# Performance work log

Hardware: AMD Instinct MI355X
Metric: run time of the kernel (lower is better)

Reference implementation:

```python
import jax, jax.numpy as jnp
import numpy as np

LOG2PI = float(np.log(2.0 * np.pi))
BATCH = 131072
IN_FEATURES = 128
MULT = 3          # Gaussian multiplicity / Sum in_channels
CARD = 2          # first Product cardinality -> 64 features


def setup_inputs() -> dict:
    key = jax.random.key(0)
    k1, k2, k3, k4, k5 = jax.random.split(key, 5)
    x = jax.random.normal(k1, (BATCH, IN_FEATURES), dtype=jnp.float32)
    means = jax.random.normal(k2, (1, IN_FEATURES, MULT), dtype=jnp.float32)
    # stds drawn positive (torch.rand init for scale params)
    stds = jax.random.uniform(k3, (1, IN_FEATURES, MULT), dtype=jnp.float32,
                              minval=0.1, maxval=1.0)
    sum_weights = jax.random.normal(k4, (64, MULT, 1), dtype=jnp.float32)
    # randomized Product layer: fixed random permutation of the 128 features
    perm = jax.random.permutation(k5, IN_FEATURES).astype(jnp.int32)
    return {"x": x, "means": means, "stds": stds,
            "sum_weights": sum_weights, "perm": perm}


def reference(x, means, stds, sum_weights, perm):
    n = x.shape[0]
    # --- Gaussian leaf: Normal(mu, sigma).log_prob(x) -> [n, 128, 3]
    z = (x[:, :, None] - means) / stds
    lp = -0.5 * (z * z) - jnp.log(stds) - 0.5 * LOG2PI
    # --- Product(in_features=128, cardinality=2, randomize): permute features,
    # pair them up, product in log-domain = sum -> [n, 64, 3]
    lp = lp[:, perm, :]
    lp = lp.reshape(n, IN_FEATURES // CARD, CARD, MULT).sum(axis=2)
    # --- Sum(in_channels=3, in_features=64, out_channels=1): weighted
    # log-sum-exp mixture over channels with log_softmax-normalized weights
    logw = jax.nn.log_softmax(sum_weights, axis=1)          # [64, 3, 1]
    lp = jax.nn.logsumexp(lp[:, :, :, None] + logw[None], axis=2)  # [n, 64, 1]
    # --- Product(in_features=64, cardinality=64): sum all features -> [n, 1, 1]
    # (permutation before a full reduction is a no-op, so omitted)
    out = lp.sum(axis=1, keepdims=True).reshape(n, 1, 1)
    return out
```

## Files before the change

### kernel.cpp

```cpp
#include <hip/hip_runtime.h>

#define N_FEAT 128
#define ROWS   32
#define TPB    256

template<int CTRL>
__device__ __forceinline__ float dpp_xadd(float v) {
    int t = __builtin_amdgcn_update_dpp(0, __float_as_int(v), CTRL, 0xF, 0xF, true);
    return v + __int_as_float(t);
}

__device__ __forceinline__ float wave_allsum(float v) {
    v = dpp_xadd<0xB1>(v);
    v = dpp_xadd<0x4E>(v);
    v = dpp_xadd<0x141>(v);
    v = dpp_xadd<0x140>(v);
#if __has_builtin(__builtin_amdgcn_permlane16_swap)
    {
        auto p = __builtin_amdgcn_permlane16_swap(__float_as_uint(v), __float_as_uint(v), false, false);
        v = __uint_as_float(p[0]) + __uint_as_float(p[1]);
    }
#else
    v += __int_as_float(__builtin_amdgcn_ds_swizzle(__float_as_int(v), 0x401F));
#endif
    {
        auto p = __builtin_amdgcn_permlane32_swap(__float_as_uint(v), __float_as_uint(v), false, false);
        v = __uint_as_float(p[0]) + __uint_as_float(p[1]);
    }
    return v;
}

__global__ __launch_bounds__(TPB, 6)
void spn_fused(const float* __restrict__ x,
               const float* __restrict__ means,
               const float* __restrict__ stds,
               const float* __restrict__ sumw,
               const int* __restrict__ perm,
               float* __restrict__ out, int n) {
    __shared__ float sx[ROWS * N_FEAT];

    const float NHALF_LOG2E = -0.7213475204444817f;
    const float LN2     = 0.6931471805599453f;
    const float LOG2PI_ = 1.8378770664093453f;
    const float LOG2E   = 1.4426950408889634f;

    const int tid  = threadIdx.x;
    const int lane = tid & 63;
    const int wv   = tid >> 6;

    const int ntiles = n / ROWS;

    auto issue_tile = [&](int t) {
        const float* g0 = x + (size_t)t * (ROWS * N_FEAT);
#pragma unroll
        for (int it = 0; it < 4; ++it) {
            const int chunk = it * 4 + wv;
            __builtin_amdgcn_global_load_lds(
                (const __attribute__((address_space(1))) unsigned*)(g0 + chunk * 256 + lane * 4),
                (__attribute__((address_space(3))) unsigned*)(sx + chunk * 256),
                16, 0, 0);
        }
    };

    int tile  = blockIdx.x;
    bool have = tile < ntiles;
    if (have) issue_tile(tile);

    const int g  = lane;
    const int p0 = perm[2 * g], p1 = perm[2 * g + 1];
    const float w0 = sumw[g * 3 + 0], w1 = sumw[g * 3 + 1], w2 = sumw[g * 3 + 2];
    const float wmx = fmaxf(w0, fmaxf(w1, w2));
    const float lse = wmx + logf(expf(w0 - wmx) + expf(w1 - wmx) + expf(w2 - wmx));
    float nm0[3], is0[3], nm1[3], is1[3], C2[3];
#pragma unroll
    for (int m = 0; m < 3; ++m) {
        const float s0 = stds[p0 * 3 + m], mu0 = means[p0 * 3 + m];
        const float s1 = stds[p1 * 3 + m], mu1 = means[p1 * 3 + m];
        const float i0 = 1.0f / s0, i1 = 1.0f / s1;
        const float wm = (m == 0 ? w0 : (m == 1 ? w1 : w2));
        nm0[m] = mu0 * i0;  is0[m] = i0;
        nm1[m] = mu1 * i1;  is1[m] = i1;
        C2[m]  = ((wm - lse) - logf(s0) - logf(s1) - LOG2PI_) * LOG2E;
    }

    while (have) {
        __syncthreads();

        const int rowbase = tile * ROWS;
        float res[8];
#pragma unroll
        for (int r = 0; r < 8; ++r) {
            const float* xr = sx + (wv * 8 + r) * N_FEAT;
            const float a = xr[p0];
            const float b = xr[p1];
            float v0, v1, v2;
            {
                float z0 = fmaf(a, is0[0], -nm0[0]);
                float z1 = fmaf(b, is1[0], -nm1[0]);
                v0 = fmaf(z0 * z0, NHALF_LOG2E, C2[0]);
                v0 = fmaf(z1 * z1, NHALF_LOG2E, v0);
            }
            {
                float z0 = fmaf(a, is0[1], -nm0[1]);
                float z1 = fmaf(b, is1[1], -nm1[1]);
                v1 = fmaf(z0 * z0, NHALF_LOG2E, C2[1]);
                v1 = fmaf(z1 * z1, NHALF_LOG2E, v1);
            }
            {
                float z0 = fmaf(a, is0[2], -nm0[2]);
                float z1 = fmaf(b, is1[2], -nm1[2]);
                v2 = fmaf(z0 * z0, NHALF_LOG2E, C2[2]);
                v2 = fmaf(z1 * z1, NHALF_LOG2E, v2);
            }
            float pmx = fmaxf(v0, fmaxf(v1, v2));
            float s = __builtin_amdgcn_exp2f(v0 - pmx)
                    + __builtin_amdgcn_exp2f(v1 - pmx)
                    + __builtin_amdgcn_exp2f(v2 - pmx);
            res[r] = pmx + __builtin_amdgcn_logf(s);
        }

#pragma unroll
        for (int r = 0; r < 8; ++r)
            res[r] = wave_allsum(res[r]);

        const int next = tile + (int)gridDim.x;
        have = next < ntiles;
        if (have) {
            __syncthreads();
            issue_tile(next);
        }

        if (lane == 0) {
            float4* op = (float4*)(out + rowbase + wv * 8);
            op[0] = make_float4(res[0] * LN2, res[1] * LN2, res[2] * LN2, res[3] * LN2);
            op[1] = make_float4(res[4] * LN2, res[5] * LN2, res[6] * LN2, res[7] * LN2);
        }
        tile = next;
    }
}

extern "C" void kernel_launch(void* const* d_in, const int* in_sizes, int n_in,
                              void* d_out, int out_size, void* d_ws, size_t ws_size,
                              hipStream_t stream) {
    const float* x     = (const float*)d_in[0];
    const float* means = (const float*)d_in[1];
    const float* stds  = (const float*)d_in[2];
    const float* sumw  = (const float*)d_in[3];
    const int*   perm  = (const int*)d_in[4];
    float* out = (float*)d_out;
    int n = in_sizes[0] / N_FEAT;

    int ntiles = n / ROWS;
    int grid = ntiles > 0 ? ntiles : 1;
    if (grid > 16384) grid = 16384;

    hipLaunchKernelGGL(spn_fused, dim3(grid), dim3(TPB), 0, stream,
                       x, means, stds, sumw, perm, out, n);
}
```

Baseline: 104.9 us.

## Double-buffer per-wave LDS tiles in a persistent grid with vmcnt waits

```diff
diff --git a/kernel.cpp b/kernel.cpp
--- a/kernel.cpp
+++ b/kernel.cpp
@@ -3,6 +3,9 @@
 #define N_FEAT 128
 #define ROWS   32
 #define TPB    256
+#define GRID   1024
+
+#define WAITV(N) asm volatile("s_waitcnt vmcnt(" #N ")" ::: "memory")
 
 template<int CTRL>
 __device__ __forceinline__ float dpp_xadd(float v) {
@@ -30,67 +33,82 @@
     return v;
 }
 
-__global__ __launch_bounds__(TPB, 6)
+__global__ __launch_bounds__(TPB, 4)
 void spn_fused(const float* __restrict__ x,
                const float* __restrict__ means,
                const float* __restrict__ stds,
                const float* __restrict__ sumw,
                const int* __restrict__ perm,
                float* __restrict__ out, int n) {
-    __shared__ float sx[ROWS * N_FEAT];
+    __shared__ float sx[2 * ROWS * N_FEAT];
 
     const float NHALF_LOG2E = -0.7213475204444817f;
-    const float LN2     = 0.6931471805599453f;
-    const float LOG2PI_ = 1.8378770664093453f;
-    const float LOG2E   = 1.4426950408889634f;
+    const float LN2      = 0.6931471805599453f;
+    const float LOG2E    = 1.4426950408889634f;
+    const float L2PI_L2E = 2.6514961294723187f;
 
     const int tid  = threadIdx.x;
     const int lane = tid & 63;
     const int wv   = tid >> 6;
 
+    float* buf0 = sx + wv * (8 * N_FEAT);
+    float* buf1 = sx + 4 * (8 * N_FEAT) + wv * (8 * N_FEAT);
+
     const int ntiles = n / ROWS;
+    const int stride = gridDim.x;
 
-    auto issue_tile = [&](int t) {
-        const float* g0 = x + (size_t)t * (ROWS * N_FEAT);
+    auto issue = [&](int t, float* dst) {
+        const float* g0 = x + (size_t)t * (ROWS * N_FEAT) + wv * (8 * N_FEAT);
 #pragma unroll
         for (int it = 0; it < 4; ++it) {
-            const int chunk = it * 4 + wv;
             __builtin_amdgcn_global_load_lds(
-                (const __attribute__((address_space(1))) unsigned*)(g0 + chunk * 256 + lane * 4),
-                (__attribute__((address_space(3))) unsigned*)(sx + chunk * 256),
+                (const __attribute__((address_space(1))) unsigned*)(g0 + it * 256 + lane * 4),
+                (__attribute__((address_space(3))) unsigned*)(dst + it * 256),
                 16, 0, 0);
         }
     };
 
-    int tile  = blockIdx.x;
-    bool have = tile < ntiles;
-    if (have) issue_tile(tile);
+    const int t0 = blockIdx.x;
+    if (t0 < ntiles) issue(t0, buf0);
 
     const int g  = lane;
     const int p0 = perm[2 * g], p1 = perm[2 * g + 1];
-    const float w0 = sumw[g * 3 + 0], w1 = sumw[g * 3 + 1], w2 = sumw[g * 3 + 2];
-    const float wmx = fmaxf(w0, fmaxf(w1, w2));
-    const float lse = wmx + logf(expf(w0 - wmx) + expf(w1 - wmx) + expf(w2 - wmx));
+    float w2[3];
+#pragma unroll
+    for (int m = 0; m < 3; ++m) w2[m] = sumw[g * 3 + m] * LOG2E;
+    const float mx2 = fmaxf(w2[0], fmaxf(w2[1], w2[2]));
+    const float lse2 = mx2 + __builtin_amdgcn_logf(__builtin_amdgcn_exp2f(w2[0] - mx2)
+                                                 + __builtin_amdgcn_exp2f(w2[1] - mx2)
+                                                 + __builtin_amdgcn_exp2f(w2[2] - mx2));
     float nm0[3], is0[3], nm1[3], is1[3], C2[3];
 #pragma unroll
     for (int m = 0; m < 3; ++m) {
         const float s0 = stds[p0 * 3 + m], mu0 = means[p0 * 3 + m];
         const float s1 = stds[p1 * 3 + m], mu1 = means[p1 * 3 + m];
         const float i0 = 1.0f / s0, i1 = 1.0f / s1;
-        const float wm = (m == 0 ? w0 : (m == 1 ? w1 : w2));
         nm0[m] = mu0 * i0;  is0[m] = i0;
         nm1[m] = mu1 * i1;  is1[m] = i1;
-        C2[m]  = ((wm - lse) - logf(s0) - logf(s1) - LOG2PI_) * LOG2E;
+        C2[m]  = (w2[m] - lse2) - __builtin_amdgcn_logf(s0)
+                                - __builtin_amdgcn_logf(s1) - L2PI_L2E;
     }
 
-    while (have) {
-        __syncthreads();
+    WAITV(0);
 
-        const int rowbase = tile * ROWS;
+    int k = 0;
+    for (int t = t0; t < ntiles; t += stride, ++k) {
+        float* cbuf = (k & 1) ? buf1 : buf0;
+        const int tn = t + stride;
+        if (tn < ntiles) {
+            issue(tn, (k & 1) ? buf0 : buf1);
+            WAITV(6);
+        } else {
+            WAITV(2);
+        }
+
         float res[8];
 #pragma unroll
         for (int r = 0; r < 8; ++r) {
-            const float* xr = sx + (wv * 8 + r) * N_FEAT;
+            const float* xr = cbuf + r * N_FEAT;
             const float a = xr[p0];
             const float b = xr[p1];
             float v0, v1, v2;
@@ -123,19 +141,11 @@
         for (int r = 0; r < 8; ++r)
             res[r] = wave_allsum(res[r]);
 
-        const int next = tile + (int)gridDim.x;
-        have = next < ntiles;
-        if (have) {
-            __syncthreads();
-            issue_tile(next);
-        }
-
         if (lane == 0) {
-            float4* op = (float4*)(out + rowbase + wv * 8);
+            float4* op = (float4*)(out + t * ROWS + wv * 8);
             op[0] = make_float4(res[0] * LN2, res[1] * LN2, res[2] * LN2, res[3] * LN2);
             op[1] = make_float4(res[4] * LN2, res[5] * LN2, res[6] * LN2, res[7] * LN2);
         }
-        tile = next;
     }
 }
 
@@ -151,8 +161,7 @@
     int n = in_sizes[0] / N_FEAT;
 
     int ntiles = n / ROWS;
-    int grid = ntiles > 0 ? ntiles : 1;
-    if (grid > 16384) grid = 16384;
+    int grid = GRID < ntiles ? GRID : (ntiles > 0 ? ntiles : 1);
 
     hipLaunchKernelGGL(spn_fused, dim3(grid), dim3(TPB), 0, stream,
                        x, means, stds, sumw, perm, out, n);
```

New measurement: 99.82 us. 4.8% less time.
